# Performance work log

Hardware: AMD Instinct MI355X
Metric: run time of the kernel (lower is better)

The kernel has to match this reference:

```python
import jax, jax.numpy as jnp
import numpy as np

B, T, F_DIM = 256, 96, 368
D_MODEL = min(768, F_DIM)   # d_model = min(hidden_dim, feat_dim)
NUM_CLASSES = 29
WINDOW = 5


def setup_inputs() -> dict:
    key = jax.random.key(0)
    ks = jax.random.split(key, 12)
    s_in = 1.0 / np.sqrt(F_DIM)
    s_h = 1.0 / np.sqrt(D_MODEL)
    return {
        "features": jax.random.normal(ks[0], (B, T, F_DIM), jnp.float32),
        "hand": jax.random.uniform(ks[1], (B, 2), jnp.float32),
        # single-layer GRU params (torch layout: (3H, in) / (3H, H))
        "gru_Wi": jax.random.normal(ks[2], (3 * D_MODEL, F_DIM), jnp.float32) * s_in,
        "gru_Wh": jax.random.normal(ks[3], (3 * D_MODEL, D_MODEL), jnp.float32) * s_h,
        "gru_bi": jax.random.normal(ks[4], (3 * D_MODEL,), jnp.float32) * s_h,
        "gru_bh": jax.random.normal(ks[5], (3 * D_MODEL,), jnp.float32) * s_h,
        # coarse predictor: Linear(d_model, 2)
        "Wc": jax.random.normal(ks[6], (2, D_MODEL), jnp.float32) * s_h,
        "bc": jax.random.normal(ks[7], (2,), jnp.float32) * s_h,
        # fine predictor: Linear(d_model, num_classes)
        "Wf": jax.random.normal(ks[8], (NUM_CLASSES, D_MODEL), jnp.float32) * s_h,
        "bf": jax.random.normal(ks[9], (NUM_CLASSES,), jnp.float32) * s_h,
    }


def _gru(x, Wi, Wh, bi, bh):
    """Single-layer unidirectional GRU (torch gate math). x: (B,T,F) -> (B,T,H)."""
    H = Wh.shape[1]
    xproj = jnp.einsum("btf,gf->btg", x, Wi) + bi  # (B,T,3H)

    def step(h, xt):
        gi_r, gi_z, gi_n = jnp.split(xt, 3, axis=-1)
        gh = h @ Wh.T + bh
        gh_r, gh_z, gh_n = jnp.split(gh, 3, axis=-1)
        r = jax.nn.sigmoid(gi_r + gh_r)
        z = jax.nn.sigmoid(gi_z + gh_z)
        n = jnp.tanh(gi_n + r * gh_n)
        h_new = (1.0 - z) * n + z * h
        return h_new, h_new

    h0 = jnp.zeros((x.shape[0], H), x.dtype)
    _, hs = jax.lax.scan(step, h0, jnp.swapaxes(xproj, 0, 1))  # (T,B,H)
    return jnp.swapaxes(hs, 0, 1)


def _apply_nms(scores):
    """Vectorized version of the per-position sliding-window min suppression.
    scores: (B,T,2). Keep row i iff scores[:, i, 0] equals the min of its
    window of size WINDOW (clipped at sequence boundaries)."""
    bg = scores[..., 0]  # (B,T)
    half = WINDOW // 2
    padded = jnp.pad(bg, ((0, 0), (half, half)), constant_values=jnp.inf)
    Tlen = bg.shape[1]
    shifts = jnp.stack([padded[:, k:k + Tlen] for k in range(WINDOW)], axis=0)
    wmin = jnp.min(shifts, axis=0)  # (B,T)
    keep = (bg == wmin)[..., None]
    return jnp.where(keep, scores, jnp.zeros_like(scores))


def reference(features, hand, gru_Wi, gru_Wh, gru_bi, gru_bh, Wc, bc, Wf, bf):
    # hand is accepted (matching the torch forward signature) but unused there too.
    temporal = _gru(features, gru_Wi, gru_Wh, gru_bi, gru_bh)  # (B,T,D)
    coarse_logits = temporal @ Wc.T + bc                        # (B,T,2)
    fine_logits = temporal @ Wf.T + bf                          # (B,T,C)
    coarse_scores = jax.nn.softmax(coarse_logits, axis=2)
    fine_scores = jax.nn.sigmoid(fine_logits)
    coarse_nms = _apply_nms(coarse_scores)
    coarse_decisions = jnp.argmax(coarse_nms, axis=2)
    return coarse_decisions, coarse_nms, fine_scores
```

## Files before the change

kernel.cpp:

```cpp
#include <hip/hip_runtime.h>
#include <hip/hip_bf16.h>

#define B_ 256
#define T_ 96
#define F_ 368
#define H_ 368
#define G3_ 1104
#define NC_ 29
#define BT_ (B_*T_)
#define HB_ (H_*B_)

#define NSL 8
#define NU 46
#define NCOL 138
#define ROWS 8
#define WQCOLS 1152

#define WQ2_U16 (8*9*12*2*64*8)

#define SENT 0x7FC07FC0u

#define F4C(v, i) ((i)==0?(v).x:((i)==1?(v).y:((i)==2?(v).z:(v).w)))

typedef __attribute__((ext_vector_type(8))) short bhalf8;
typedef __attribute__((ext_vector_type(4))) float f32x4;

__device__ __forceinline__ unsigned short f2bf(float x) {
    unsigned u = __float_as_uint(x);
    u += 0x7fffu + ((u >> 16) & 1u);
    return (unsigned short)(u >> 16);
}
__device__ __forceinline__ float bf2f(unsigned short b) {
    return __uint_as_float(((unsigned)b) << 16);
}

__device__ __forceinline__ void gll16(const void* g, void* l) {
    __builtin_amdgcn_global_load_lds(
        (const __attribute__((address_space(1))) void*)g,
        (__attribute__((address_space(3))) void*)l, 16, 0, 0);
}

__device__ __forceinline__ unsigned int bload_u(const unsigned int* p) {
    return __hip_atomic_load(p, __ATOMIC_RELAXED, __HIP_MEMORY_SCOPE_AGENT);
}
__device__ __forceinline__ void bstore_u(unsigned int* p, unsigned int v) {
    __hip_atomic_store(p, v, __ATOMIC_RELAXED, __HIP_MEMORY_SCOPE_AGENT);
}
__device__ __forceinline__ unsigned long long bload_u2(const unsigned long long* p) {
    return __hip_atomic_load(p, __ATOMIC_RELAXED, __HIP_MEMORY_SCOPE_AGENT);
}

__device__ __forceinline__ void barrier_lds() {
    asm volatile("s_waitcnt lgkmcnt(0)\ns_barrier" ::: "memory");
}

__global__ __launch_bounds__(256) void k_prep_wq2(const float* __restrict__ Wh,
                                                  unsigned short* __restrict__ Wq2) {
    const int idx = blockIdx.x*256 + threadIdx.x;
    const int l = idx & 63;
    const int p = (idx >> 6) & 1;
    int q = idx >> 7;
    const int kt = q % 12; q /= 12;
    const int nt = q % 9;
    const int us = q / 9;
    const int col = nt*16 + (l & 15);
    const int k0 = kt*32 + (l >> 4)*8;
    float v[8];
    #pragma unroll
    for (int e = 0; e < 8; ++e) v[e] = 0.f;
    if (col < NCOL && k0 < H_) {
        const int g = col / NU, uu = col - g*NU;
        const int grow = g*H_ + us*NU + uu;
        const float4 f0 = *reinterpret_cast<const float4*>(Wh + (size_t)grow*H_ + k0);
        const float4 f1 = *reinterpret_cast<const float4*>(Wh + (size_t)grow*H_ + k0 + 4);
        v[0]=f0.x; v[1]=f0.y; v[2]=f0.z; v[3]=f0.w;
        v[4]=f1.x; v[5]=f1.y; v[6]=f1.z; v[7]=f1.w;
    }
    unsigned int o[4];
    #pragma unroll
    for (int e = 0; e < 4; ++e) {
        const unsigned short h0 = f2bf(v[2*e]), h1 = f2bf(v[2*e+1]);
        const unsigned short w0 = p ? f2bf(v[2*e]   - bf2f(h0)) : h0;
        const unsigned short w1 = p ? f2bf(v[2*e+1] - bf2f(h1)) : h1;
        o[e] = (unsigned)w0 | ((unsigned)w1 << 16);
    }
    uint4* dst = reinterpret_cast<uint4*>(Wq2 + (size_t)idx*8);
    *dst = make_uint4(o[0], o[1], o[2], o[3]);
}

__global__ __launch_bounds__(256) void k_prep_wcat(const float* __restrict__ Wc,
                                                   const float* __restrict__ Wf,
                                                   float* __restrict__ Wcat) {
    const int idx = blockIdx.x*256 + threadIdx.x;
    const int u = idx >> 5, c = idx & 31;
    float v = 0.f;
    if (c < 2) v = Wc[c*H_ + u];
    else if (c < 31) v = Wf[(c-2)*H_ + u];
    Wcat[idx] = v;
}

__global__ __launch_bounds__(256) void k_fill_sent(unsigned int* __restrict__ p) {
    const int idx = blockIdx.x*256 + threadIdx.x;
    reinterpret_cast<uint4*>(p)[idx] = make_uint4(SENT, SENT, SENT, SENT);
}

__global__ __launch_bounds__(256) void k_split_a(const float* __restrict__ src,
                                                 unsigned short* __restrict__ Ah,
                                                 unsigned short* __restrict__ Al) {
    const int idx = blockIdx.x*256 + threadIdx.x;
    const float4 v = reinterpret_cast<const float4*>(src)[idx];
    ushort4 h, lo;
    h.x = f2bf(v.x); lo.x = f2bf(v.x - bf2f(h.x));
    h.y = f2bf(v.y); lo.y = f2bf(v.y - bf2f(h.y));
    h.z = f2bf(v.z); lo.z = f2bf(v.z - bf2f(h.z));
    h.w = f2bf(v.w); lo.w = f2bf(v.w - bf2f(h.w));
    reinterpret_cast<ushort4*>(Ah)[idx] = h;
    reinterpret_cast<ushort4*>(Al)[idx] = lo;
}

__global__ __launch_bounds__(256) void k_split_b(const float* __restrict__ Wi,
                                                 unsigned short* __restrict__ Bh,
                                                 unsigned short* __restrict__ Bl) {
    const int idx = blockIdx.x*256 + threadIdx.x;
    const float x = (idx < G3_*F_) ? Wi[idx] : 0.f;
    const unsigned short h = f2bf(x);
    Bh[idx] = h;
    Bl[idx] = f2bf(x - bf2f(h));
}

__global__ __launch_bounds__(256) void k_xproj_mfma(
        const unsigned short* __restrict__ Ah, const unsigned short* __restrict__ Al,
        const unsigned short* __restrict__ Bh, const unsigned short* __restrict__ Bl,
        const float* __restrict__ bias, float* __restrict__ C)
{
    __shared__ unsigned short sAh[128*32], sAl[128*32], sBh[128*32], sBl[128*32];
    const int tid = threadIdx.x;
    const int w   = tid >> 6, l = tid & 63;
    const int gm0 = blockIdx.y * 128, gn0 = blockIdx.x * 128;

    const int srow = tid >> 2;
    const int cg   = (tid & 3) ^ ((tid >> 3) & 3);
    const size_t aoff0 = (size_t)(gm0 + srow)      * F_ + cg * 8;
    const size_t aoff1 = (size_t)(gm0 + srow + 64) * F_ + cg * 8;
    const size_t boff0 = (size_t)(gn0 + srow)      * F_ + cg * 8;
    const size_t boff1 = (size_t)(gn0 + srow + 64) * F_ + cg * 8;
    const int lb0 = w * 1024, lb1 = 4096 + w * 1024;

    const int lr = l & 15, lk = l >> 4;
    const int cswz = (lk ^ ((lr >> 1) & 3)) * 16;
    const int wr = w >> 1, wc = w & 1;
    int offA[4], offB[4];
    #pragma unroll
    for (int f = 0; f < 4; ++f) {
        offA[f] = (wr*64 + f*16 + lr) * 64 + cswz;
        offB[f] = (wc*64 + f*16 + lr) * 64 + cswz;
    }

    f32x4 acc[4][4];
    #pragma unroll
    for (int i = 0; i < 4; ++i)
        #pragma unroll
        for (int j = 0; j < 4; ++j) acc[i][j] = f32x4{0.f,0.f,0.f,0.f};

    auto stage = [&](int kt) {
        const size_t ko = (size_t)kt * 32;
        gll16(Ah + aoff0 + ko, (char*)sAh + lb0);
        gll16(Ah + aoff1 + ko, (char*)sAh + lb1);
        gll16(Al + aoff0 + ko, (char*)sAl + lb0);
        gll16(Al + aoff1 + ko, (char*)sAl + lb1);
        gll16(Bh + boff0 + ko, (char*)sBh + lb0);
        gll16(Bh + boff1 + ko, (char*)sBh + lb1);
        gll16(Bl + boff0 + ko, (char*)sBl + lb0);
        gll16(Bl + boff1 + ko, (char*)sBl + lb1);
    };

    stage(0);
    for (int kt = 0; kt < 12; ++kt) {
        __syncthreads();
        if (kt == 11) {
            if (cg >= 2) {
                const f32x4 z = f32x4{0.f,0.f,0.f,0.f};
                *reinterpret_cast<f32x4*>((char*)sAh + tid*16)        = z;
                *reinterpret_cast<f32x4*>((char*)sAh + tid*16 + 4096) = z;
                *reinterpret_cast<f32x4*>((char*)sAl + tid*16)        = z;
                *reinterpret_cast<f32x4*>((char*)sAl + tid*16 + 4096) = z;
                *reinterpret_cast<f32x4*>((char*)sBh + tid*16)        = z;
                *reinterpret_cast<f32x4*>((char*)sBh + tid*16 + 4096) = z;
                *reinterpret_cast<f32x4*>((char*)sBl + tid*16)        = z;
                *reinterpret_cast<f32x4*>((char*)sBl + tid*16 + 4096) = z;
            }
            __syncthreads();
        }
        bhalf8 fAh[4], fAl[4], fBh[4], fBl[4];
        #pragma unroll
        for (int f = 0; f < 4; ++f) {
            fAh[f] = *reinterpret_cast<const bhalf8*>((const char*)sAh + offA[f]);
            fAl[f] = *reinterpret_cast<const bhalf8*>((const char*)sAl + offA[f]);
            fBh[f] = *reinterpret_cast<const bhalf8*>((const char*)sBh + offB[f]);
            fBl[f] = *reinterpret_cast<const bhalf8*>((const char*)sBl + offB[f]);
        }
        __syncthreads();
        if (kt < 11) stage(kt + 1);
        #pragma unroll
        for (int i = 0; i < 4; ++i)
            #pragma unroll
            for (int j = 0; j < 4; ++j) {
                acc[i][j] = __builtin_amdgcn_mfma_f32_16x16x32_bf16(fAh[i], fBh[j], acc[i][j], 0, 0, 0);
                acc[i][j] = __builtin_amdgcn_mfma_f32_16x16x32_bf16(fAh[i], fBl[j], acc[i][j], 0, 0, 0);
                acc[i][j] = __builtin_amdgcn_mfma_f32_16x16x32_bf16(fAl[i], fBh[j], acc[i][j], 0, 0, 0);
            }
    }

    #pragma unroll
    for (int j = 0; j < 4; ++j) {
        const int gcol = gn0 + wc*64 + j*16 + lr;
        if (gcol < G3_) {
            const float bv = bias[gcol];
            #pragma unroll
            for (int i = 0; i < 4; ++i) {
                const int grow = gm0 + wr*64 + i*16 + lk*4;
                float* cp = C + (size_t)grow * G3_ + gcol;
                #pragma unroll
                for (int q = 0; q < 4; ++q)
                    cp[(size_t)q * G3_] = acc[i][j][q] + bv;
            }
        }
    }
}

__global__ __launch_bounds__(512, 2) void k_gru_all(const float* __restrict__ xproj,
                                                    const unsigned short* __restrict__ Wq2,
                                                    const float* __restrict__ bh,
                                                    unsigned int* __restrict__ h2) {
    __shared__ unsigned short sAh[48*16*8];
    __shared__ unsigned short sAl[48*16*8];
    __shared__ float part2[4][144][9];
    const int tid = threadIdx.x;
    const int us  = blockIdx.x & 7;
    const int bg  = blockIdx.x >> 3;
    const int b0  = bg * ROWS;
    const int w   = tid >> 6;
    const int l   = tid & 63;
    const int wk  = w >> 1;
    const int wn  = w & 1;
    const int nt0 = wn * 4;

    for (int s = tid; s < 48*16*8; s += 512) { sAh[s] = 0; sAl[s] = 0; }
    for (int s = tid; s < 4*144*9; s += 512) (&part2[0][0][0])[s] = 0.f;

    bhalf8 bB[5][3][2];
    #pragma unroll
    for (int ti = 0; ti < 5; ++ti)
        #pragma unroll
        for (int kti = 0; kti < 3; ++kti)
            #pragma unroll
            for (int p = 0; p < 2; ++p)
                bB[ti][kti][p] = *reinterpret_cast<const bhalf8*>(
                    Wq2 + ((((size_t)(us*9 + nt0 + ti)*12 + (wk*3 + kti))*2 + p)*64 + l)*8);

    const bool gact = tid < ROWS*NU;
    const int u1 = tid % NU, r1 = tid / NU;
    const int ug1 = us*NU + u1;
    float bh1r = 0.f, bh1z = 0.f, bh1n = 0.f;
    if (gact) { bh1r = bh[ug1]; bh1z = bh[H_+ug1]; bh1n = bh[2*H_+ug1]; }

    int aoff2[3]; bool sact[3];
    #pragma unroll
    for (int ii = 0; ii < 3; ++ii) {
        const int pi = l + ii*64;
        sact[ii] = pi < 184;
        const int pc = sact[ii] ? pi : 0;
        const int u = NU*w + (pc >> 2), r2 = pc & 3;
        aoff2[ii] = ((u >> 3)*16 + 2*r2)*8 + (u & 7);
    }

    const int aoffb = (l >> 4)*256 + (l & 15)*16;

    __syncthreads();

    for (int t = 0; t < T_; ++t) {
        unsigned int* hout = h2 + ((size_t)t*32 + bg)*2944;

        float xg10 = 0.f, xg11 = 0.f, xg12 = 0.f;
        if (gact) {
            const float* xr1 = xproj + ((size_t)(b0 + r1)*T_ + t)*G3_;
            xg10 = xr1[ug1]; xg11 = xr1[H_+ug1]; xg12 = xr1[2*H_+ug1];
        }

        if (t > 0) {
            const unsigned long long* hin64 =
                reinterpret_cast<const unsigned long long*>(
                    h2 + ((size_t)(t - 1)*32 + bg)*2944) + 184*w;
            unsigned long long v[3];
            bool need[3];
            #pragma unroll
            for (int ii = 0; ii < 3; ++ii) {
                need[ii] = sact[ii];
                v[ii] = 0ull;
                if (need[ii]) v[ii] = bload_u2(hin64 + l + ii*64);
            }
            for (;;) {
                unsigned bad = 0u;
                #pragma unroll
                for (int ii = 0; ii < 3; ++ii) {
                    if (need[ii]) {
                        const bool inv = ((unsigned)v[ii] == SENT) ||
                                         ((unsigned)(v[ii] >> 32) == SENT);
                        need[ii] = inv;
                        if (inv) bad = 1u;
                    }
                }
                if (!__any(bad != 0u)) break;
                #pragma unroll
                for (int ii = 0; ii < 3; ++ii)
                    if (need[ii]) v[ii] = bload_u2(hin64 + l + ii*64);
            }
            #pragma unroll
            for (int ii = 0; ii < 3; ++ii) {
                if (sact[ii]) {
                    const unsigned int v0 = (unsigned int)v[ii];
                    const unsigned int v1 = (unsigned int)(v[ii] >> 32);
                    const int a = aoff2[ii];
                    sAh[a]     = (unsigned short)(v0 & 0xffffu);
                    sAl[a]     = (unsigned short)(v0 >> 16);
                    sAh[a + 8] = (unsigned short)(v1 & 0xffffu);
                    sAl[a + 8] = (unsigned short)(v1 >> 16);
                }
            }
            barrier_lds();
            f32x4 acc[5];
            #pragma unroll
            for (int ti = 0; ti < 5; ++ti) acc[ti] = f32x4{0.f,0.f,0.f,0.f};
            #pragma unroll
            for (int kti = 0; kti < 3; ++kti) {
                const int kt = wk*3 + kti;
                const bhalf8 fh = *reinterpret_cast<const bhalf8*>((const char*)sAh + kt*1024 + aoffb);
                const bhalf8 fl = *reinterpret_cast<const bhalf8*>((const char*)sAl + kt*1024 + aoffb);
                #pragma unroll
                for (int ti = 0; ti < 5; ++ti) {
                    acc[ti] = __builtin_amdgcn_mfma_f32_16x16x32_bf16(fh, bB[ti][kti][0], acc[ti], 0, 0, 0);
                    acc[ti] = __builtin_amdgcn_mfma_f32_16x16x32_bf16(fh, bB[ti][kti][1], acc[ti], 0, 0, 0);
                    acc[ti] = __builtin_amdgcn_mfma_f32_16x16x32_bf16(fl, bB[ti][kti][0], acc[ti], 0, 0, 0);
                }
            }
            if (l < 32) {
                #pragma unroll
                for (int ti = 0; ti < 5; ++ti) {
                    const int col = (nt0 + ti)*16 + (l & 15);
                    float* pp = &part2[wk][col][(l >> 4)*4];
                    pp[0] = acc[ti][0]; pp[1] = acc[ti][1];
                    pp[2] = acc[ti][2]; pp[3] = acc[ti][3];
                }
            }
        }
        barrier_lds();

        if (gact) {
            float s0 = 0.f, s1 = 0.f, s2 = 0.f;
            #pragma unroll
            for (int q2 = 0; q2 < 4; ++q2) {
                s0 += part2[q2][u1][r1];
                s1 += part2[q2][NU + u1][r1];
                s2 += part2[q2][2*NU + u1][r1];
            }
            const float rg = 1.f/(1.f + expf(-(xg10 + s0 + bh1r)));
            const float zg = 1.f/(1.f + expf(-(xg11 + s1 + bh1z)));
            const float ng = tanhf(xg12 + rg*(s2 + bh1n));
            float hp = 0.f;
            if (t > 0) {
                const int a = ((ug1 >> 3)*16 + r1)*8 + (ug1 & 7);
                hp = bf2f(sAh[a]) + bf2f(sAl[a]);
            }
            const float hn = (1.f - zg)*ng + zg*hp;
            const unsigned short hi = f2bf(hn);
            const unsigned short lo = f2bf(hn - bf2f(hi));
            bstore_u(hout + ug1*8 + r1, (unsigned)hi | ((unsigned)lo << 16));
        }
        barrier_lds();
    }
}

__global__ __launch_bounds__(256) void k_heads2(const unsigned int* __restrict__ temporal2,
                                                const float* __restrict__ Wcat,
                                                const float* __restrict__ bc,
                                                const float* __restrict__ bf,
                                                float* __restrict__ cs,
                                                float* __restrict__ fine_out) {
    const int t = blockIdx.x;
    const int b = threadIdx.x;
    const unsigned int* tb = temporal2 + (size_t)t*HB_ + (b >> 3)*2944 + (b & 7);
    float acc[31];
    #pragma unroll
    for (int c = 0; c < 31; ++c) acc[c] = 0.f;
    for (int u = 0; u < H_; ++u) {
        const unsigned int v = tb[(size_t)u*8];
        const float x = bf2f((unsigned short)(v & 0xffffu)) + bf2f((unsigned short)(v >> 16));
        const float* wrow = Wcat + u*32;
        #pragma unroll
        for (int c = 0; c < 31; ++c) acc[c] = fmaf(x, wrow[c], acc[c]);
    }
    const float l0 = acc[0] + bc[0], l1 = acc[1] + bc[1];
    const float m  = fmaxf(l0, l1);
    const float e0 = expf(l0 - m), e1 = expf(l1 - m);
    const float inv = 1.f/(e0 + e1);
    cs[((size_t)b*T_ + t)*2]     = e0*inv;
    cs[((size_t)b*T_ + t)*2 + 1] = e1*inv;
    #pragma unroll
    for (int c = 2; c < 31; ++c) {
        fine_out[((size_t)b*T_ + t)*NC_ + (c-2)] = 1.f/(1.f + expf(-(acc[c] + bf[c-2])));
    }
}

__global__ __launch_bounds__(256) void k_nms(const float* __restrict__ cs,
                                             float* __restrict__ out_dec,
                                             float* __restrict__ out_nms) {
    const int idx = blockIdx.x*256 + threadIdx.x;
    const int t = idx % T_;
    const float bg = cs[idx*2], s1 = cs[idx*2+1];
    float wmin = bg;
    #pragma unroll
    for (int dt = -2; dt <= 2; ++dt) {
        const int tt = t + dt;
        if (dt != 0 && tt >= 0 && tt < T_) wmin = fminf(wmin, cs[(idx + dt)*2]);
    }
    const bool keep = (bg <= wmin);
    out_dec[idx]     = (keep && (s1 > bg)) ? 1.f : 0.f;
    out_nms[idx*2]   = keep ? bg : 0.f;
    out_nms[idx*2+1] = keep ? s1 : 0.f;
}

extern "C" void kernel_launch(void* const* d_in, const int* in_sizes, int n_in,
                              void* d_out, int out_size, void* d_ws, size_t ws_size,
                              hipStream_t stream) {
    const float* features = (const float*)d_in[0];
    const float* Wi = (const float*)d_in[2];
    const float* Wh = (const float*)d_in[3];
    const float* bi = (const float*)d_in[4];
    const float* bh = (const float*)d_in[5];
    const float* Wc = (const float*)d_in[6];
    const float* bc = (const float*)d_in[7];
    const float* Wf = (const float*)d_in[8];
    const float* bf = (const float*)d_in[9];

    float* out = (float*)d_out;
    float* out_dec  = out;
    float* out_nms  = out + BT_;
    float* out_fine = out + BT_ + 2*BT_;

    float* xproj = (float*)d_ws;
    unsigned short* Wq2 = (unsigned short*)(xproj + (size_t)BT_*G3_);
    unsigned int* temporal2 = (unsigned int*)((char*)Wq2 + (size_t)WQ2_U16*2);
    float* Wcat = xproj;
    float* cs   = xproj + 12288;

    unsigned short* Bh16 = (unsigned short*)Wq2;
    unsigned short* Bl16 = Bh16 + (size_t)WQCOLS*F_;
    unsigned short* Ah16 = (unsigned short*)temporal2;
    unsigned short* Al16 = Ah16 + (size_t)BT_*F_;

    k_split_a<<<8832, 256, 0, stream>>>(features, Ah16, Al16);
    k_split_b<<<1656, 256, 0, stream>>>(Wi, Bh16, Bl16);
    k_xproj_mfma<<<dim3(9, 192), 256, 0, stream>>>(Ah16, Al16, Bh16, Bl16, bi, xproj);
    k_prep_wq2<<<432, 256, 0, stream>>>(Wh, Wq2);
    k_fill_sent<<<8832, 256, 0, stream>>>(temporal2);
    k_gru_all<<<256, 512, 0, stream>>>(xproj, Wq2, bh, temporal2);
    k_prep_wcat<<<46, 256, 0, stream>>>(Wc, Wf, Wcat);
    k_heads2<<<96, 256, 0, stream>>>(temporal2, Wcat, bc, bf, cs, out_fine);
    k_nms<<<96, 256, 0, stream>>>(cs, out_dec, out_nms);
}
```

Before: 597.7 us.

## Double-buffer GRU hidden state in LDS, skip self-slice polling, transpose xproj

The GRU kernel now keeps the hidden state in two LDS buffers. Each block writes its own slice locally, so the wave matching its own slice (w == us) no longer polls global memory for data it produced itself. The xproj GEMM writes its output in time-major order, so the per-step loads of the input projection are contiguous across batch rows. Block-to-(slice, batch-group) mapping is also remapped so blocks sharing a batch group are spread differently across CUs. This adds LDS usage and strided writes in the GEMM epilogue.

```diff
diff --git a/kernel.cpp b/kernel.cpp
--- a/kernel.cpp
+++ b/kernel.cpp
@@ -20,8 +20,6 @@
 
 #define SENT 0x7FC07FC0u
 
-#define F4C(v, i) ((i)==0?(v).x:((i)==1?(v).y:((i)==2?(v).z:(v).w)))
-
 typedef __attribute__((ext_vector_type(8))) short bhalf8;
 typedef __attribute__((ext_vector_type(4))) float f32x4;
 
@@ -40,9 +38,6 @@
         (__attribute__((address_space(3))) void*)l, 16, 0, 0);
 }
 
-__device__ __forceinline__ unsigned int bload_u(const unsigned int* p) {
-    return __hip_atomic_load(p, __ATOMIC_RELAXED, __HIP_MEMORY_SCOPE_AGENT);
-}
 __device__ __forceinline__ void bstore_u(unsigned int* p, unsigned int v) {
     __hip_atomic_store(p, v, __ATOMIC_RELAXED, __HIP_MEMORY_SCOPE_AGENT);
 }
@@ -219,25 +214,27 @@
             #pragma unroll
             for (int i = 0; i < 4; ++i) {
                 const int grow = gm0 + wr*64 + i*16 + lk*4;
-                float* cp = C + (size_t)grow * G3_ + gcol;
                 #pragma unroll
-                for (int q = 0; q < 4; ++q)
-                    cp[(size_t)q * G3_] = acc[i][j][q] + bv;
-            }
-        }
-    }
-}
-
-__global__ __launch_bounds__(512, 2) void k_gru_all(const float* __restrict__ xproj,
+                for (int q = 0; q < 4; ++q) {
+                    const int m = grow + q;
+                    const int bq = m / T_, tq = m - bq*T_;
+                    C[((size_t)tq*B_ + bq)*G3_ + gcol] = acc[i][j][q] + bv;
+                }
+            }
+        }
+    }
+}
+
+__global__ __launch_bounds__(512, 2) void k_gru_all(const float* __restrict__ xprojT,
                                                     const unsigned short* __restrict__ Wq2,
                                                     const float* __restrict__ bh,
                                                     unsigned int* __restrict__ h2) {
-    __shared__ unsigned short sAh[48*16*8];
-    __shared__ unsigned short sAl[48*16*8];
+    __shared__ unsigned short sAh[2][6144];
+    __shared__ unsigned short sAl[2][6144];
     __shared__ float part2[4][144][9];
     const int tid = threadIdx.x;
-    const int us  = blockIdx.x & 7;
-    const int bg  = blockIdx.x >> 3;
+    const int us  = blockIdx.x >> 5;
+    const int bg  = blockIdx.x & 31;
     const int b0  = bg * ROWS;
     const int w   = tid >> 6;
     const int l   = tid & 63;
@@ -245,7 +242,9 @@
     const int wn  = w & 1;
     const int nt0 = wn * 4;
 
-    for (int s = tid; s < 48*16*8; s += 512) { sAh[s] = 0; sAl[s] = 0; }
+    for (int s = tid; s < 6144; s += 512) {
+        sAh[0][s] = 0; sAh[1][s] = 0; sAl[0][s] = 0; sAl[1][s] = 0;
+    }
     for (int s = tid; s < 4*144*9; s += 512) (&part2[0][0][0])[s] = 0.f;
 
     bhalf8 bB[5][3][2];
@@ -261,6 +260,7 @@
     const bool gact = tid < ROWS*NU;
     const int u1 = tid % NU, r1 = tid / NU;
     const int ug1 = us*NU + u1;
+    const int ga  = ((ug1 >> 3)*16 + r1)*8 + (ug1 & 7);
     float bh1r = 0.f, bh1z = 0.f, bh1n = 0.f;
     if (gact) { bh1r = bh[ug1]; bh1z = bh[H_+ug1]; bh1n = bh[2*H_+ug1]; }
 
@@ -279,52 +279,56 @@
     __syncthreads();
 
     for (int t = 0; t < T_; ++t) {
+        const int rb = (t - 1) & 1;
+        const int wb = t & 1;
         unsigned int* hout = h2 + ((size_t)t*32 + bg)*2944;
 
         float xg10 = 0.f, xg11 = 0.f, xg12 = 0.f;
         if (gact) {
-            const float* xr1 = xproj + ((size_t)(b0 + r1)*T_ + t)*G3_;
-            xg10 = xr1[ug1]; xg11 = xr1[H_+ug1]; xg12 = xr1[2*H_+ug1];
+            const float* xp = xprojT + ((size_t)t*B_ + b0 + r1)*G3_;
+            xg10 = xp[ug1]; xg11 = xp[H_+ug1]; xg12 = xp[2*H_+ug1];
         }
 
         if (t > 0) {
-            const unsigned long long* hin64 =
-                reinterpret_cast<const unsigned long long*>(
-                    h2 + ((size_t)(t - 1)*32 + bg)*2944) + 184*w;
-            unsigned long long v[3];
-            bool need[3];
-            #pragma unroll
-            for (int ii = 0; ii < 3; ++ii) {
-                need[ii] = sact[ii];
-                v[ii] = 0ull;
-                if (need[ii]) v[ii] = bload_u2(hin64 + l + ii*64);
-            }
-            for (;;) {
-                unsigned bad = 0u;
+            if (w != us) {
+                const unsigned long long* hin64 =
+                    reinterpret_cast<const unsigned long long*>(
+                        h2 + ((size_t)(t - 1)*32 + bg)*2944) + 184*w;
+                unsigned long long v[3];
+                bool need[3];
                 #pragma unroll
                 for (int ii = 0; ii < 3; ++ii) {
-                    if (need[ii]) {
-                        const bool inv = ((unsigned)v[ii] == SENT) ||
-                                         ((unsigned)(v[ii] >> 32) == SENT);
-                        need[ii] = inv;
-                        if (inv) bad = 1u;
+                    need[ii] = sact[ii];
+                    v[ii] = 0ull;
+                    if (need[ii]) v[ii] = bload_u2(hin64 + l + ii*64);
+                }
+                for (;;) {
+                    unsigned bad = 0u;
+                    #pragma unroll
+                    for (int ii = 0; ii < 3; ++ii) {
+                        if (need[ii]) {
+                            const bool inv = ((unsigned)v[ii] == SENT) ||
+                                             ((unsigned)(v[ii] >> 32) == SENT);
+                            need[ii] = inv;
+                            if (inv) bad = 1u;
+                        }
                     }
-                }
-                if (!__any(bad != 0u)) break;
+                    if (!__any(bad != 0u)) break;
+                    #pragma unroll
+                    for (int ii = 0; ii < 3; ++ii)
+                        if (need[ii]) v[ii] = bload_u2(hin64 + l + ii*64);
+                }
                 #pragma unroll
-                for (int ii = 0; ii < 3; ++ii)
-                    if (need[ii]) v[ii] = bload_u2(hin64 + l + ii*64);
-            }
-            #pragma unroll
-            for (int ii = 0; ii < 3; ++ii) {
-                if (sact[ii]) {
-                    const unsigned int v0 = (unsigned int)v[ii];
-                    const unsigned int v1 = (unsigned int)(v[ii] >> 32);
-                    const int a = aoff2[ii];
-                    sAh[a]     = (unsigned short)(v0 & 0xffffu);
-                    sAl[a]     = (unsigned short)(v0 >> 16);
-                    sAh[a + 8] = (unsigned short)(v1 & 0xffffu);
-                    sAl[a + 8] = (unsigned short)(v1 >> 16);
+                for (int ii = 0; ii < 3; ++ii) {
+                    if (sact[ii]) {
+                        const unsigned int v0 = (unsigned int)v[ii];
+                        const unsigned int v1 = (unsigned int)(v[ii] >> 32);
+                        const int a = aoff2[ii];
+                        sAh[rb][a]     = (unsigned short)(v0 & 0xffffu);
+                        sAl[rb][a]     = (unsigned short)(v0 >> 16);
+                        sAh[rb][a + 8] = (unsigned short)(v1 & 0xffffu);
+                        sAl[rb][a + 8] = (unsigned short)(v1 >> 16);
+                    }
                 }
             }
             barrier_lds();
@@ -334,8 +338,10 @@
             #pragma unroll
             for (int kti = 0; kti < 3; ++kti) {
                 const int kt = wk*3 + kti;
-                const bhalf8 fh = *reinterpret_cast<const bhalf8*>((const char*)sAh + kt*1024 + aoffb);
-                const bhalf8 fl = *reinterpret_cast<const bhalf8*>((const char*)sAl + kt*1024 + aoffb);
+                const bhalf8 fh = *reinterpret_cast<const bhalf8*>(
+                    (const char*)sAh[rb] + kt*1024 + aoffb);
+                const bhalf8 fl = *reinterpret_cast<const bhalf8*>(
+                    (const char*)sAl[rb] + kt*1024 + aoffb);
                 #pragma unroll
                 for (int ti = 0; ti < 5; ++ti) {
                     acc[ti] = __builtin_amdgcn_mfma_f32_16x16x32_bf16(fh, bB[ti][kti][0], acc[ti], 0, 0, 0);
@@ -367,13 +373,11 @@
             const float zg = 1.f/(1.f + expf(-(xg11 + s1 + bh1z)));
             const float ng = tanhf(xg12 + rg*(s2 + bh1n));
             float hp = 0.f;
-            if (t > 0) {
-                const int a = ((ug1 >> 3)*16 + r1)*8 + (ug1 & 7);
-                hp = bf2f(sAh[a]) + bf2f(sAl[a]);
-            }
+            if (t > 0) hp = bf2f(sAh[rb][ga]) + bf2f(sAl[rb][ga]);
             const float hn = (1.f - zg)*ng + zg*hp;
             const unsigned short hi = f2bf(hn);
             const unsigned short lo = f2bf(hn - bf2f(hi));
+            sAh[wb][ga] = hi; sAl[wb][ga] = lo;
             bstore_u(hout + ug1*8 + r1, (unsigned)hi | ((unsigned)lo << 16));
         }
         barrier_lds();
@@ -447,11 +451,11 @@
     float* out_nms  = out + BT_;
     float* out_fine = out + BT_ + 2*BT_;
 
-    float* xproj = (float*)d_ws;
-    unsigned short* Wq2 = (unsigned short*)(xproj + (size_t)BT_*G3_);
+    float* xprojT = (float*)d_ws;
+    unsigned short* Wq2 = (unsigned short*)(xprojT + (size_t)BT_*G3_);
     unsigned int* temporal2 = (unsigned int*)((char*)Wq2 + (size_t)WQ2_U16*2);
-    float* Wcat = xproj;
-    float* cs   = xproj + 12288;
+    float* Wcat = xprojT;
+    float* cs   = xprojT + 12288;
 
     unsigned short* Bh16 = (unsigned short*)Wq2;
     unsigned short* Bl16 = Bh16 + (size_t)WQCOLS*F_;
@@ -460,10 +464,10 @@
 
     k_split_a<<<8832, 256, 0, stream>>>(features, Ah16, Al16);
     k_split_b<<<1656, 256, 0, stream>>>(Wi, Bh16, Bl16);
-    k_xproj_mfma<<<dim3(9, 192), 256, 0, stream>>>(Ah16, Al16, Bh16, Bl16, bi, xproj);
+    k_xproj_mfma<<<dim3(9, 192), 256, 0, stream>>>(Ah16, Al16, Bh16, Bl16, bi, xprojT);
     k_prep_wq2<<<432, 256, 0, stream>>>(Wh, Wq2);
     k_fill_sent<<<8832, 256, 0, stream>>>(temporal2);
-    k_gru_all<<<256, 512, 0, stream>>>(xproj, Wq2, bh, temporal2);
+    k_gru_all<<<256, 512, 0, stream>>>(xprojT, Wq2, bh, temporal2);
     k_prep_wcat<<<46, 256, 0, stream>>>(Wc, Wf, Wcat);
     k_heads2<<<96, 256, 0, stream>>>(temporal2, Wcat, bc, bf, cs, out_fine);
     k_nms<<<96, 256, 0, stream>>>(cs, out_dec, out_nms);
```

Result: slower. 728.5 us (+21.9%).
